# Kernel optimization log

Hardware: AMD Instinct MI355X
Metric: run time of the kernel (lower is better)

Reference implementation:

```python
import jax, jax.numpy as jnp
import numpy as np

# Module constants (from init_kwargs): 2D domain, m=[1024,1024], omega=[0,1,0,1]
PAD = 2
M0, M1 = 1024, 1024
OMEGA_LO = np.array([0.0, 0.0], dtype=np.float32)   # omega[0::2]
H = np.array([1.0 / 1024.0, 1.0 / 1024.0], dtype=np.float32)  # (omega_hi-omega_lo)/m
N_POINTS = 2097152


def _b0(j, xi):
    # Cubic B-spline basis pieces, exactly as SplineInter.b0
    if j == 1:
        return (2 + xi) * (2 + xi) * (2 + xi)
    elif j == 2:
        return -(3 * xi + 6) * (xi * xi) + 4
    elif j == 3:
        return (3 * xi - 6) * (xi * xi) + 4
    elif j == 4:
        return (2 - xi) * (2 - xi) * (2 - xi)


def _basis(t):
    # t: [N] fractional part; returns [N,4] weights for offsets j=-1,0,1,2
    # matches b0(3 - j, t - j)
    return jnp.stack([_b0(3 - j, t - j) for j in range(-1, 3)], axis=-1)


def setup_inputs() -> dict:
    key = jax.random.key(0)
    k1, k2 = jax.random.split(key)
    # query points in physical domain [0,1)^2 -> normalized coords in [-0.5, 1023.5)
    x = jax.random.uniform(k1, (N_POINTS, 2), dtype=jnp.float32)
    # padded spline coefficient grid: (M0+2*PAD, M1+2*PAD)
    coeffs = 0.1 * jax.random.normal(k2, (M0 + 2 * PAD, M1 + 2 * PAD), dtype=jnp.float32)
    return {"x": x, "coeffs": coeffs}


def reference(x, coeffs):
    x = x.reshape(-1, 2)
    # normalize to grid coords
    xn = (x - jnp.asarray(OMEGA_LO)) / jnp.asarray(H) - 0.5  # [N,2]
    m = jnp.array([M0, M1], dtype=xn.dtype)
    valid = jnp.all((xn > -2) & (xn < m), axis=1)            # [N]
    P = jnp.floor(xn).astype(jnp.int32)                      # [N,2]
    t = xn - P                                               # fractional part [N,2]

    i1 = M1 + 2 * PAD  # row stride of padded coeff grid
    p = i1 * (PAD + P[:, 0]) + (PAD + P[:, 1])               # [N] base flat index

    w0 = _basis(t[:, 0])  # [N,4]
    w1 = _basis(t[:, 1])  # [N,4]

    js = jnp.arange(-1, 3, dtype=jnp.int32)
    idx = p[:, None, None] + js[:, None] * i1 + js[None, :]  # [N,4,4]
    cflat = coeffs.reshape(-1)
    safe_idx = jnp.clip(idx, 0, cflat.shape[0] - 1)
    vals = cflat[safe_idx]                                   # [N,4,4] gathered stencil

    out = jnp.einsum('nij,ni,nj->n', vals, w0, w1)
    out = jnp.where(valid, out, 0.0)
    return out[:, None]  # [N,1]
```

## Files before the change

kernel.cpp:

```cpp
#include <hip/hip_runtime.h>


#define I1 1028
#define TOTAL (1028 * 1028)
#define NQI 257
#define COPY_ELEMS (NQI * I1)
#define NCOPIES 4
#define QTOT (NCOPIES * COPY_ELEMS)

typedef float f4u __attribute__((ext_vector_type(4), aligned(4)));

__device__ __forceinline__ void basis4(float t, float w[4]) {
    float a = 1.0f - t;
    w[0] = a * a * a;
    w[1] = (3.0f * t - 6.0f) * (t * t) + 4.0f;
    float xi = t - 1.0f;
    w[2] = -(3.0f * xi + 6.0f) * (xi * xi) + 4.0f;
    w[3] = t * t * t;
}

struct PointSetup {
    int base;
    int r0, c0;
    bool valid;
    bool qinterior;
    float w0[4], w1[4];
};

__device__ __forceinline__ PointSetup setup_point(float px, float py) {
    PointSetup ps;
    float xn0 = px * 1024.0f - 0.5f;
    float xn1 = py * 1024.0f - 0.5f;

    ps.valid = (xn0 > -2.0f) && (xn0 < 1024.0f) &&
               (xn1 > -2.0f) && (xn1 < 1024.0f);

    float P0f = floorf(xn0);
    float P1f = floorf(xn1);
    int P0 = (int)P0f;
    int P1 = (int)P1f;
    float t0 = xn0 - P0f;
    float t1 = xn1 - P1f;

    basis4(t0, ps.w0);
    basis4(t1, ps.w1);

    ps.base = I1 * (2 + P0) + (2 + P1);
    ps.r0 = P0 + 1;
    ps.c0 = P1 + 1;
    ps.qinterior = (ps.r0 >= 0) && (ps.r0 <= 1024) &&
                   (ps.c0 >= 0) && (ps.c0 <= 1024);
    return ps;
}

__device__ __forceinline__ float eval_slow(const float* __restrict__ coeffs,
                                           const PointSetup& ps) {
    float acc = 0.0f;
#pragma unroll
    for (int j = 0; j < 4; ++j) {
        int r = ps.base + (j - 1) * I1 - 1;
        float s = 0.0f;
#pragma unroll
        for (int k = 0; k < 4; ++k) {
            int idx = r + k;
            idx = min(max(idx, 0), TOTAL - 1);
            s = fmaf(coeffs[idx], ps.w1[k], s);
        }
        acc = fmaf(s, ps.w0[j], acc);
    }
    return acc;
}

__device__ __forceinline__ float reduce_phase(const float4 v[4], const PointSetup& ps) {
    float acc = 0.0f;
#pragma unroll
    for (int k = 0; k < 4; ++k) {
        float col = fmaf(v[k].x, ps.w0[0],
                    fmaf(v[k].y, ps.w0[1],
                    fmaf(v[k].z, ps.w0[2],
                         v[k].w * ps.w0[3])));
        acc = fmaf(col, ps.w1[k], acc);
    }
    return acc;
}


__global__ __launch_bounds__(256) void phasepack_kernel(
    const float* __restrict__ coeffs, float4* __restrict__ Q)
{
    int idx = blockIdx.x * blockDim.x + threadIdx.x;
    if (idx >= QTOT) return;
    int p   = idx / COPY_ELEMS;
    int rem = idx - p * COPY_ELEMS;
    int i   = rem / I1;
    int c   = rem - i * I1;
    int r   = 4 * i + p;
    int r0 = min(r,     1027);
    int r1 = min(r + 1, 1027);
    int r2 = min(r + 2, 1027);
    int r3 = min(r + 3, 1027);
    float4 v;
    v.x = coeffs[r0 * I1 + c];
    v.y = coeffs[r1 * I1 + c];
    v.z = coeffs[r2 * I1 + c];
    v.w = coeffs[r3 * I1 + c];
    Q[idx] = v;
}


__global__ __launch_bounds__(256) void eval_phase_kernel(
    const float* __restrict__ x,
    const float* __restrict__ coeffs,
    const float4* __restrict__ Q,
    float* __restrict__ out, int n)
{
    int g = blockIdx.x * blockDim.x + threadIdx.x;
    int i0 = 2 * g;
    if (i0 >= n) return;

    if (i0 + 1 < n) {
        float4 two = reinterpret_cast<const float4*>(x)[g];
        PointSetup psA = setup_point(two.x, two.y);
        PointSetup psB = setup_point(two.z, two.w);

        float accA, accB;
        if (psA.qinterior && psB.qinterior) {
            const float4* qA = Q + (psA.r0 & 3) * COPY_ELEMS
                                 + (psA.r0 >> 2) * I1 + psA.c0;
            const float4* qB = Q + (psB.r0 & 3) * COPY_ELEMS
                                 + (psB.r0 >> 2) * I1 + psB.c0;
            float4 vA[4], vB[4];
#pragma unroll
            for (int k = 0; k < 4; ++k) {
                vA[k] = qA[k];
                vB[k] = qB[k];
            }
            accA = reduce_phase(vA, psA);
            accB = reduce_phase(vB, psB);
        } else {
            accA = eval_slow(coeffs, psA);
            accB = eval_slow(coeffs, psB);
        }

        float2 o;
        o.x = psA.valid ? accA : 0.0f;
        o.y = psB.valid ? accB : 0.0f;
        reinterpret_cast<float2*>(out)[g] = o;
    } else {
        float px = x[2 * i0], py = x[2 * i0 + 1];
        PointSetup ps = setup_point(px, py);
        float acc = eval_slow(coeffs, ps);
        out[i0] = ps.valid ? acc : 0.0f;
    }
}


__global__ __launch_bounds__(256) void spline_interp_kernel(
    const float* __restrict__ x,
    const float* __restrict__ coeffs,
    float* __restrict__ out,
    int n, int half)
{
    int i = blockIdx.x * blockDim.x + threadIdx.x;
    if (i >= half) return;
    int i2 = i + half;

    float2 xyA = reinterpret_cast<const float2*>(x)[i];
    float2 xyB = reinterpret_cast<const float2*>(x)[i2];

    PointSetup psA = setup_point(xyA.x, xyA.y);
    PointSetup psB = setup_point(xyB.x, xyB.y);

    float accA, accB;
    bool interiorA = (psA.base - I1 - 1 >= 0) && (psA.base + 2 * I1 + 2 <= TOTAL - 1);
    bool interiorB = (psB.base - I1 - 1 >= 0) && (psB.base + 2 * I1 + 2 <= TOTAL - 1);
    if (interiorA && interiorB) {
        f4u vA[4], vB[4];
#pragma unroll
        for (int j = 0; j < 4; ++j) {
            vA[j] = *reinterpret_cast<const f4u*>(coeffs + psA.base + (j - 1) * I1 - 1);
            vB[j] = *reinterpret_cast<const f4u*>(coeffs + psB.base + (j - 1) * I1 - 1);
        }
        float a0 = 0.0f, a1 = 0.0f;
#pragma unroll
        for (int j = 0; j < 4; ++j) {
            float s0 = fmaf(vA[j].x, psA.w1[0], fmaf(vA[j].y, psA.w1[1],
                       fmaf(vA[j].z, psA.w1[2], vA[j].w * psA.w1[3])));
            a0 = fmaf(s0, psA.w0[j], a0);
            float s1 = fmaf(vB[j].x, psB.w1[0], fmaf(vB[j].y, psB.w1[1],
                       fmaf(vB[j].z, psB.w1[2], vB[j].w * psB.w1[3])));
            a1 = fmaf(s1, psB.w0[j], a1);
        }
        accA = a0; accB = a1;
    } else {
        accA = eval_slow(coeffs, psA);
        accB = eval_slow(coeffs, psB);
    }

    out[i]  = psA.valid ? accA : 0.0f;
    out[i2] = psB.valid ? accB : 0.0f;
}


extern "C" void kernel_launch(void* const* d_in, const int* in_sizes, int n_in,
                              void* d_out, int out_size, void* d_ws, size_t ws_size,
                              hipStream_t stream) {
    const float* x = (const float*)d_in[0];
    const float* coeffs = (const float*)d_in[1];
    float* out = (float*)d_out;

    int n = in_sizes[0] / 2;

    size_t need = (size_t)QTOT * 16;

    if (ws_size >= need) {
        float4* Q = (float4*)d_ws;

        int gpack = (QTOT + 255) / 256;
        phasepack_kernel<<<gpack, 256, 0, stream>>>(coeffs, Q);

        int pairs = (n + 1) / 2;
        int geval = (pairs + 255) / 256;
        eval_phase_kernel<<<geval, 256, 0, stream>>>(x, coeffs, Q, out, n);
    } else {
        int half = n / 2;
        int block = 256;
        int grid = (half + block - 1) / block;
        spline_interp_kernel<<<grid, block, 0, stream>>>(x, coeffs, out, n, half);
    }
}
```

Baseline: 111.1 us.

## Pack coefficients into 16 phase copies of aligned 4x4 tiles

```diff
diff --git a/kernel.cpp b/kernel.cpp
--- a/kernel.cpp
+++ b/kernel.cpp
@@ -3,10 +3,10 @@
 
 #define I1 1028
 #define TOTAL (1028 * 1028)
-#define NQI 257
-#define COPY_ELEMS (NQI * I1)
-#define NCOPIES 4
-#define QTOT (NCOPIES * COPY_ELEMS)
+#define NGRP 257
+#define LINES_PER_COPY (NGRP * NGRP)
+#define NCOPIES 16
+#define NLINES (NCOPIES * LINES_PER_COPY)
 
 typedef float f4u __attribute__((ext_vector_type(4), aligned(4)));
 
@@ -71,7 +71,7 @@
     return acc;
 }
 
-__device__ __forceinline__ float reduce_phase(const float4 v[4], const PointSetup& ps) {
+__device__ __forceinline__ float reduce_tile(const float4 v[4], const PointSetup& ps) {
     float acc = 0.0f;
 #pragma unroll
     for (int k = 0; k < 4; ++k) {
@@ -85,30 +85,40 @@
 }
 
 
-__global__ __launch_bounds__(256) void phasepack_kernel(
+__global__ __launch_bounds__(256) void tilepack_kernel(
     const float* __restrict__ coeffs, float4* __restrict__ Q)
 {
     int idx = blockIdx.x * blockDim.x + threadIdx.x;
-    if (idx >= QTOT) return;
-    int p   = idx / COPY_ELEMS;
-    int rem = idx - p * COPY_ELEMS;
-    int i   = rem / I1;
-    int c   = rem - i * I1;
-    int r   = 4 * i + p;
-    int r0 = min(r,     1027);
-    int r1 = min(r + 1, 1027);
-    int r2 = min(r + 2, 1027);
-    int r3 = min(r + 3, 1027);
-    float4 v;
-    v.x = coeffs[r0 * I1 + c];
-    v.y = coeffs[r1 * I1 + c];
-    v.z = coeffs[r2 * I1 + c];
-    v.w = coeffs[r3 * I1 + c];
-    Q[idx] = v;
-}
-
-
-__global__ __launch_bounds__(256) void eval_phase_kernel(
+    if (idx >= NLINES) return;
+    int pq  = idx / LINES_PER_COPY;
+    int rem = idx - pq * LINES_PER_COPY;
+    int i   = rem / NGRP;
+    int j   = rem - i * NGRP;
+    int p   = pq >> 2;
+    int q   = pq & 3;
+
+    int rb = 4 * i + p;
+    int cb = 4 * j + q;
+    int r0 = min(rb,     1027);
+    int r1 = min(rb + 1, 1027);
+    int r2 = min(rb + 2, 1027);
+    int r3 = min(rb + 3, 1027);
+
+    float4* dst = Q + (size_t)idx * 4;
+#pragma unroll
+    for (int k = 0; k < 4; ++k) {
+        int c = min(cb + k, 1027);
+        float4 v;
+        v.x = coeffs[r0 * I1 + c];
+        v.y = coeffs[r1 * I1 + c];
+        v.z = coeffs[r2 * I1 + c];
+        v.w = coeffs[r3 * I1 + c];
+        dst[k] = v;
+    }
+}
+
+
+__global__ __launch_bounds__(256) void eval_tile_kernel(
     const float* __restrict__ x,
     const float* __restrict__ coeffs,
     const float4* __restrict__ Q,
@@ -125,18 +135,20 @@
 
         float accA, accB;
         if (psA.qinterior && psB.qinterior) {
-            const float4* qA = Q + (psA.r0 & 3) * COPY_ELEMS
-                                 + (psA.r0 >> 2) * I1 + psA.c0;
-            const float4* qB = Q + (psB.r0 & 3) * COPY_ELEMS
-                                 + (psB.r0 >> 2) * I1 + psB.c0;
+            int lineA = (((psA.r0 & 3) * 4 + (psA.c0 & 3)) * NGRP
+                         + (psA.r0 >> 2)) * NGRP + (psA.c0 >> 2);
+            int lineB = (((psB.r0 & 3) * 4 + (psB.c0 & 3)) * NGRP
+                         + (psB.r0 >> 2)) * NGRP + (psB.c0 >> 2);
+            const float4* qA = Q + (size_t)lineA * 4;
+            const float4* qB = Q + (size_t)lineB * 4;
             float4 vA[4], vB[4];
 #pragma unroll
             for (int k = 0; k < 4; ++k) {
                 vA[k] = qA[k];
                 vB[k] = qB[k];
             }
-            accA = reduce_phase(vA, psA);
-            accB = reduce_phase(vB, psB);
+            accA = reduce_tile(vA, psA);
+            accB = reduce_tile(vB, psB);
         } else {
             accA = eval_slow(coeffs, psA);
             accB = eval_slow(coeffs, psB);
@@ -211,17 +223,17 @@
 
     int n = in_sizes[0] / 2;
 
-    size_t need = (size_t)QTOT * 16;
+    size_t need = (size_t)NLINES * 64;
 
     if (ws_size >= need) {
         float4* Q = (float4*)d_ws;
 
-        int gpack = (QTOT + 255) / 256;
-        phasepack_kernel<<<gpack, 256, 0, stream>>>(coeffs, Q);
+        int gpack = (NLINES + 255) / 256;
+        tilepack_kernel<<<gpack, 256, 0, stream>>>(coeffs, Q);
 
         int pairs = (n + 1) / 2;
         int geval = (pairs + 255) / 256;
-        eval_phase_kernel<<<geval, 256, 0, stream>>>(x, coeffs, Q, out, n);
+        eval_tile_kernel<<<geval, 256, 0, stream>>>(x, coeffs, Q, out, n);
     } else {
         int half = n / 2;
         int block = 256;
```

Measured after the change: 132.9 us. 1.2x slower.

## Drop phase-packed coefficient copy; one point per thread with direct row loads

Applied to the files above, without the earlier changes.

```diff
diff --git a/kernel.cpp b/kernel.cpp
--- a/kernel.cpp
+++ b/kernel.cpp
@@ -3,10 +3,6 @@
 
 #define I1 1028
 #define TOTAL (1028 * 1028)
-#define NQI 257
-#define COPY_ELEMS (NQI * I1)
-#define NCOPIES 4
-#define QTOT (NCOPIES * COPY_ELEMS)
 
 typedef float f4u __attribute__((ext_vector_type(4), aligned(4)));
 
@@ -19,21 +15,22 @@
     w[3] = t * t * t;
 }
 
-struct PointSetup {
-    int base;
-    int r0, c0;
-    bool valid;
-    bool qinterior;
-    float w0[4], w1[4];
-};
+__global__ __launch_bounds__(256) void spline_1pt_kernel(
+    const float* __restrict__ x,
+    const float* __restrict__ coeffs,
+    float* __restrict__ out,
+    int n)
+{
+    int i = blockIdx.x * blockDim.x + threadIdx.x;
+    if (i >= n) return;
 
-__device__ __forceinline__ PointSetup setup_point(float px, float py) {
-    PointSetup ps;
-    float xn0 = px * 1024.0f - 0.5f;
-    float xn1 = py * 1024.0f - 0.5f;
+    float2 xy = reinterpret_cast<const float2*>(x)[i];
 
-    ps.valid = (xn0 > -2.0f) && (xn0 < 1024.0f) &&
-               (xn1 > -2.0f) && (xn1 < 1024.0f);
+    float xn0 = xy.x * 1024.0f - 0.5f;
+    float xn1 = xy.y * 1024.0f - 0.5f;
+
+    bool valid = (xn0 > -2.0f) && (xn0 < 1024.0f) &&
+                 (xn1 > -2.0f) && (xn1 < 1024.0f);
 
     float P0f = floorf(xn0);
     float P1f = floorf(xn1);
@@ -42,165 +39,54 @@
     float t0 = xn0 - P0f;
     float t1 = xn1 - P1f;
 
-    basis4(t0, ps.w0);
-    basis4(t1, ps.w1);
+    int base = I1 * (2 + P0) + (2 + P1);
+    int r0 = P0 + 1;
+    int c0 = P1 + 1;
+    bool interior = (r0 >= 0) && (r0 <= 1024) && (c0 >= 0) && (c0 <= 1024);
 
-    ps.base = I1 * (2 + P0) + (2 + P1);
-    ps.r0 = P0 + 1;
-    ps.c0 = P1 + 1;
-    ps.qinterior = (ps.r0 >= 0) && (ps.r0 <= 1024) &&
-                   (ps.c0 >= 0) && (ps.c0 <= 1024);
-    return ps;
-}
+    float acc;
+    if (interior) {
+        const float* rowp = coeffs + base - I1 - 1;
+        f4u v0 = *reinterpret_cast<const f4u*>(rowp);
+        f4u v1 = *reinterpret_cast<const f4u*>(rowp + I1);
+        f4u v2 = *reinterpret_cast<const f4u*>(rowp + 2 * I1);
+        f4u v3 = *reinterpret_cast<const f4u*>(rowp + 3 * I1);
 
-__device__ __forceinline__ float eval_slow(const float* __restrict__ coeffs,
-                                           const PointSetup& ps) {
-    float acc = 0.0f;
+        float w0[4], w1[4];
+        basis4(t0, w0);
+        basis4(t1, w1);
+
+        float s0 = fmaf(v0.x, w1[0], fmaf(v0.y, w1[1],
+                   fmaf(v0.z, w1[2], v0.w * w1[3])));
+        float s1 = fmaf(v1.x, w1[0], fmaf(v1.y, w1[1],
+                   fmaf(v1.z, w1[2], v1.w * w1[3])));
+        float s2 = fmaf(v2.x, w1[0], fmaf(v2.y, w1[1],
+                   fmaf(v2.z, w1[2], v2.w * w1[3])));
+        float s3 = fmaf(v3.x, w1[0], fmaf(v3.y, w1[1],
+                   fmaf(v3.z, w1[2], v3.w * w1[3])));
+
+        acc = fmaf(s0, w0[0], fmaf(s1, w0[1], fmaf(s2, w0[2], s3 * w0[3])));
+    } else {
+        float w0[4], w1[4];
+        basis4(t0, w0);
+        basis4(t1, w1);
+        acc = 0.0f;
 #pragma unroll
-    for (int j = 0; j < 4; ++j) {
-        int r = ps.base + (j - 1) * I1 - 1;
-        float s = 0.0f;
-#pragma unroll
-        for (int k = 0; k < 4; ++k) {
-            int idx = r + k;
-            idx = min(max(idx, 0), TOTAL - 1);
-            s = fmaf(coeffs[idx], ps.w1[k], s);
-        }
-        acc = fmaf(s, ps.w0[j], acc);
-    }
-    return acc;
-}
-
-__device__ __forceinline__ float reduce_phase(const float4 v[4], const PointSetup& ps) {
-    float acc = 0.0f;
-#pragma unroll
-    for (int k = 0; k < 4; ++k) {
-        float col = fmaf(v[k].x, ps.w0[0],
-                    fmaf(v[k].y, ps.w0[1],
-                    fmaf(v[k].z, ps.w0[2],
-                         v[k].w * ps.w0[3])));
-        acc = fmaf(col, ps.w1[k], acc);
-    }
-    return acc;
-}
-
-
-__global__ __launch_bounds__(256) void phasepack_kernel(
-    const float* __restrict__ coeffs, float4* __restrict__ Q)
-{
-    int idx = blockIdx.x * blockDim.x + threadIdx.x;
-    if (idx >= QTOT) return;
-    int p   = idx / COPY_ELEMS;
-    int rem = idx - p * COPY_ELEMS;
-    int i   = rem / I1;
-    int c   = rem - i * I1;
-    int r   = 4 * i + p;
-    int r0 = min(r,     1027);
-    int r1 = min(r + 1, 1027);
-    int r2 = min(r + 2, 1027);
-    int r3 = min(r + 3, 1027);
-    float4 v;
-    v.x = coeffs[r0 * I1 + c];
-    v.y = coeffs[r1 * I1 + c];
-    v.z = coeffs[r2 * I1 + c];
-    v.w = coeffs[r3 * I1 + c];
-    Q[idx] = v;
-}
-
-
-__global__ __launch_bounds__(256) void eval_phase_kernel(
-    const float* __restrict__ x,
-    const float* __restrict__ coeffs,
-    const float4* __restrict__ Q,
-    float* __restrict__ out, int n)
-{
-    int g = blockIdx.x * blockDim.x + threadIdx.x;
-    int i0 = 2 * g;
-    if (i0 >= n) return;
-
-    if (i0 + 1 < n) {
-        float4 two = reinterpret_cast<const float4*>(x)[g];
-        PointSetup psA = setup_point(two.x, two.y);
-        PointSetup psB = setup_point(two.z, two.w);
-
-        float accA, accB;
-        if (psA.qinterior && psB.qinterior) {
-            const float4* qA = Q + (psA.r0 & 3) * COPY_ELEMS
-                                 + (psA.r0 >> 2) * I1 + psA.c0;
-            const float4* qB = Q + (psB.r0 & 3) * COPY_ELEMS
-                                 + (psB.r0 >> 2) * I1 + psB.c0;
-            float4 vA[4], vB[4];
+        for (int j = 0; j < 4; ++j) {
+            int r = base + (j - 1) * I1 - 1;
+            float s = 0.0f;
 #pragma unroll
             for (int k = 0; k < 4; ++k) {
-                vA[k] = qA[k];
-                vB[k] = qB[k];
+                int idx = r + k;
+                idx = min(max(idx, 0), TOTAL - 1);
+                s = fmaf(coeffs[idx], w1[k], s);
             }
-            accA = reduce_phase(vA, psA);
-            accB = reduce_phase(vB, psB);
-        } else {
-            accA = eval_slow(coeffs, psA);
-            accB = eval_slow(coeffs, psB);
+            acc = fmaf(s, w0[j], acc);
         }
-
-        float2 o;
-        o.x = psA.valid ? accA : 0.0f;
-        o.y = psB.valid ? accB : 0.0f;
-        reinterpret_cast<float2*>(out)[g] = o;
-    } else {
-        float px = x[2 * i0], py = x[2 * i0 + 1];
-        PointSetup ps = setup_point(px, py);
-        float acc = eval_slow(coeffs, ps);
-        out[i0] = ps.valid ? acc : 0.0f;
-    }
-}
-
-
-__global__ __launch_bounds__(256) void spline_interp_kernel(
-    const float* __restrict__ x,
-    const float* __restrict__ coeffs,
-    float* __restrict__ out,
-    int n, int half)
-{
-    int i = blockIdx.x * blockDim.x + threadIdx.x;
-    if (i >= half) return;
-    int i2 = i + half;
-
-    float2 xyA = reinterpret_cast<const float2*>(x)[i];
-    float2 xyB = reinterpret_cast<const float2*>(x)[i2];
-
-    PointSetup psA = setup_point(xyA.x, xyA.y);
-    PointSetup psB = setup_point(xyB.x, xyB.y);
-
-    float accA, accB;
-    bool interiorA = (psA.base - I1 - 1 >= 0) && (psA.base + 2 * I1 + 2 <= TOTAL - 1);
-    bool interiorB = (psB.base - I1 - 1 >= 0) && (psB.base + 2 * I1 + 2 <= TOTAL - 1);
-    if (interiorA && interiorB) {
-        f4u vA[4], vB[4];
-#pragma unroll
-        for (int j = 0; j < 4; ++j) {
-            vA[j] = *reinterpret_cast<const f4u*>(coeffs + psA.base + (j - 1) * I1 - 1);
-            vB[j] = *reinterpret_cast<const f4u*>(coeffs + psB.base + (j - 1) * I1 - 1);
-        }
-        float a0 = 0.0f, a1 = 0.0f;
-#pragma unroll
-        for (int j = 0; j < 4; ++j) {
-            float s0 = fmaf(vA[j].x, psA.w1[0], fmaf(vA[j].y, psA.w1[1],
-                       fmaf(vA[j].z, psA.w1[2], vA[j].w * psA.w1[3])));
-            a0 = fmaf(s0, psA.w0[j], a0);
-            float s1 = fmaf(vB[j].x, psB.w1[0], fmaf(vB[j].y, psB.w1[1],
-                       fmaf(vB[j].z, psB.w1[2], vB[j].w * psB.w1[3])));
-            a1 = fmaf(s1, psB.w0[j], a1);
-        }
-        accA = a0; accB = a1;
-    } else {
-        accA = eval_slow(coeffs, psA);
-        accB = eval_slow(coeffs, psB);
     }
 
-    out[i]  = psA.valid ? accA : 0.0f;
-    out[i2] = psB.valid ? accB : 0.0f;
+    out[i] = valid ? acc : 0.0f;
 }
-
 
 extern "C" void kernel_launch(void* const* d_in, const int* in_sizes, int n_in,
                               void* d_out, int out_size, void* d_ws, size_t ws_size,
@@ -211,21 +97,7 @@
 
     int n = in_sizes[0] / 2;
 
-    size_t need = (size_t)QTOT * 16;
-
-    if (ws_size >= need) {
-        float4* Q = (float4*)d_ws;
-
-        int gpack = (QTOT + 255) / 256;
-        phasepack_kernel<<<gpack, 256, 0, stream>>>(coeffs, Q);
-
-        int pairs = (n + 1) / 2;
-        int geval = (pairs + 255) / 256;
-        eval_phase_kernel<<<geval, 256, 0, stream>>>(x, coeffs, Q, out, n);
-    } else {
-        int half = n / 2;
-        int block = 256;
-        int grid = (half + block - 1) / block;
-        spline_interp_kernel<<<grid, block, 0, stream>>>(x, coeffs, out, n, half);
-    }
+    int block = 256;
+    int grid = (n + block - 1) / block;
+    spline_1pt_kernel<<<grid, block, 0, stream>>>(x, coeffs, out, n);
 }
```

Result: no change. 110.8 us (-0.3%).
